# Performance work log

Hardware: AMD Instinct MI355X
Metric: run time of the kernel (lower is better)

Reference implementation:

```python
import jax, jax.numpy as jnp
import numpy as np

EPS = 1e-8
PAD = 1  # kernel // 2 for kernel=3


def setup_inputs() -> dict:
    key = jax.random.key(0)
    k1, k2, k3, k4, k5 = jax.random.split(key, 5)
    b, c, h, w = 16, 256, 64, 64
    out_ch, kernel, style_dim = 256, 3, 512
    x = jax.random.normal(k1, (b, c, h, w), dtype=jnp.float32)
    style = jax.random.normal(k2, (b, style_dim), dtype=jnp.float32)
    # learned params
    weight = jax.random.normal(k3, (1, out_ch, c, kernel, kernel), dtype=jnp.float32)
    lim = 1.0 / np.sqrt(style_dim)
    mod_w = jax.random.uniform(k4, (c, style_dim), minval=-lim, maxval=lim, dtype=jnp.float32)
    mod_b = jax.random.uniform(k5, (c,), minval=-lim, maxval=lim, dtype=jnp.float32)
    return {"x": x, "style": style, "weight": weight, "mod_w": mod_w, "mod_b": mod_b}


def reference(x, style, weight, mod_w, mod_b):
    # s[b,i]: per-sample, per-input-channel modulation from the style Linear
    s = style @ mod_w.T + mod_b                     # [b, in_ch]
    w = weight[0]                                    # [out_ch, in_ch, k, k]
    # demod factor: sum_{i,kh,kw} (w[o,i,kh,kw]*s[b,i])^2 = sum_i s^2 * sum_kk w^2
    w_sq = jnp.sum(w * w, axis=(2, 3))               # [out_ch, in_ch]
    d = jax.lax.rsqrt(jnp.einsum('oi,bi->bo', w_sq, s * s) + EPS)  # [b, out_ch]
    # modulate input channels instead of materializing per-sample weights
    xs = x * s[:, :, None, None]                     # [b, in_ch, h, w]
    y = jax.lax.conv_general_dilated(
        xs, w, window_strides=(1, 1), padding=[(PAD, PAD), (PAD, PAD)],
        dimension_numbers=('NCHW', 'OIHW', 'NCHW'))
    return y * d[:, :, None, None]                   # [b, out_ch, h, w]
```

## Files before the change

### kernel.cpp

```cpp
#include <hip/hip_runtime.h>
#include <hip/hip_bf16.h>
#include <cstdint>
#include <cstddef>

typedef __bf16 bf16_t;
typedef __bf16 bf16x4 __attribute__((ext_vector_type(4)));
typedef __bf16 bf16x8 __attribute__((ext_vector_type(8)));
typedef float  f32x4  __attribute__((ext_vector_type(4)));

#define NB   16
#define NC   256
#define NO   256
#define SD   512
#define NPIX 4096
#define CPAD 36

#define WS_S   0
#define WS_D   16384
#define WS_WSQ 32768
#define WS_WT  294912

__global__ __launch_bounds__(256) void prep1(
    const float* __restrict__ style, const float* __restrict__ weight,
    const float* __restrict__ mod_w, const float* __restrict__ mod_b,
    float* __restrict__ s_buf, float* __restrict__ wsq, bf16_t* __restrict__ wT)
{
    const int blk = blockIdx.x;
    const int tid = threadIdx.x;
    if (blk < 16) {
        const int b = blk, i = tid;
        const float* st = style + b * SD;
        const float* mw = mod_w + i * SD;
        float acc = 0.f;
        for (int k = 0; k < SD; k += 4) {
            float4 a = *(const float4*)(st + k);
            float4 c = *(const float4*)(mw + k);
            acc += a.x * c.x + a.y * c.y + a.z * c.z + a.w * c.w;
        }
        s_buf[b * NC + i] = acc + mod_b[i];
    } else {
        const int o = blk - 16, i = tid;
        const float* wp = weight + (o * NC + i) * 9;
        float q = 0.f;
        #pragma unroll
        for (int t = 0; t < 9; ++t) {
            float v = wp[t];
            q += v * v;
            wT[t * (NO * NC) + o * NC + i] = (bf16_t)v;
        }
        wsq[o * NC + i] = q;
    }
}

__global__ __launch_bounds__(256) void prep2(
    const float* __restrict__ s_buf, const float* __restrict__ wsq,
    float* __restrict__ d_buf)
{
    const int b = blockIdx.x, o = threadIdx.x;
    const float* wq = wsq + o * NC;
    const float* sb = s_buf + b * NC;
    float sum = 0.f;
    for (int i = 0; i < NC; ++i) {
        float sv = sb[i];
        sum += wq[i] * sv * sv;
    }
    d_buf[b * NC + o] = rsqrtf(sum + 1e-8f);
}

__device__ __forceinline__ void stage_a(const bf16_t* __restrict__ wT_tap,
                                        int o0, int ic0, bf16_t* dst, int tid)
{
    #pragma unroll
    for (int it = 0; it < 2; ++it) {
        int s = it * 256 + tid;
        const bf16_t* g = wT_tap + (o0 + (s >> 2)) * NC + ic0 + (s & 3) * 8;
        __builtin_amdgcn_global_load_lds(
            (const __attribute__((address_space(1))) void*)g,
            (__attribute__((address_space(3))) void*)(dst + s * 8),
            16, 0, 0);
    }
}

__global__ __launch_bounds__(256) void conv_mfma(
    const float* __restrict__ x,
    const bf16_t* __restrict__ wT,
    const float* __restrict__ s_buf,
    const float* __restrict__ d_buf,
    float* __restrict__ out)
{
    __shared__ bf16_t lds_a[2][128 * 32];
    __shared__ bf16_t lds_b[4 * 64 * CPAD];

    const int tid   = threadIdx.x;
    const int lane  = tid & 63;
    const int wv    = tid >> 6;
    const int wo    = wv >> 1;
    const int wp    = wv & 1;
    const int pt    = blockIdx.x;
    const int o0    = blockIdx.y * 128;
    const int batch = blockIdx.z;
    const int row0  = pt * 2;

    const int l15 = lane & 15;
    const int k0  = (lane >> 4) * 8;

    const int colB = tid & 63;
    const int cgrp = tid >> 6;

    f32x4 acc[4][4];
    #pragma unroll
    for (int i = 0; i < 4; ++i)
        #pragma unroll
        for (int j = 0; j < 4; ++j) {
            f32x4 z = {0.f, 0.f, 0.f, 0.f};
            acc[i][j] = z;
        }

    bf16x8 bzero;
    #pragma unroll
    for (int j = 0; j < 8; ++j) bzero[j] = (bf16_t)0.f;

    for (int chunk = 0; chunk < 8; ++chunk) {
        const int ic0 = chunk * 32;

        {
            float sv[8];
            #pragma unroll
            for (int c = 0; c < 8; ++c)
                sv[c] = s_buf[batch * NC + ic0 + cgrp * 8 + c];
            const float* xbase = x + (size_t)(batch * NC + ic0 + cgrp * 8) * NPIX + colB;
            #pragma unroll
            for (int r = 0; r < 4; ++r) {
                const int gy = row0 - 1 + r;
                const bool valid = ((unsigned)gy < 64u);
                const int lbase = (r * 64 + colB) * CPAD + cgrp * 8;
                #pragma unroll
                for (int cp = 0; cp < 4; ++cp) {
                    float v0 = 0.f, v1 = 0.f;
                    if (valid) {
                        v0 = xbase[(2 * cp)     * NPIX + gy * 64] * sv[2 * cp];
                        v1 = xbase[(2 * cp + 1) * NPIX + gy * 64] * sv[2 * cp + 1];
                    }
                    union { bf16_t h[2]; uint32_t u; } pk;
                    pk.h[0] = (bf16_t)v0;
                    pk.h[1] = (bf16_t)v1;
                    *(uint32_t*)&lds_b[lbase + 2 * cp] = pk.u;
                }
            }
        }
        stage_a(wT, o0, ic0, &lds_a[0][0], tid);
        __syncthreads();

        #pragma unroll
        for (int tap = 0; tap < 9; ++tap) {
            if (tap < 8)
                stage_a(wT + (tap + 1) * (NO * NC), o0, ic0,
                        &lds_a[(tap + 1) & 1][0], tid);

            const bf16_t* abuf = &lds_a[tap & 1][0];
            const int kh = tap / 3, kw = tap % 3;

            bf16x8 af[4];
            #pragma unroll
            for (int of = 0; of < 4; ++of)
                af[of] = *(const bf16x8*)&abuf[(wo * 64 + of * 16 + l15) * 32 + k0];

            const int r = wp + kh;
            bf16x8 bfr[4];
            #pragma unroll
            for (int nf = 0; nf < 4; ++nf) {
                const int c = nf * 16 + l15 + kw - 1;
                if ((unsigned)c < 64u) {
                    const bf16_t* p = &lds_b[(r * 64 + c) * CPAD + k0];
                    bf16x4 lo = *(const bf16x4*)p;
                    bf16x4 hi = *(const bf16x4*)(p + 4);
                    bfr[nf] = __builtin_shufflevector(lo, hi, 0, 1, 2, 3, 4, 5, 6, 7);
                } else {
                    bfr[nf] = bzero;
                }
            }

            #pragma unroll
            for (int of = 0; of < 4; ++of)
                #pragma unroll
                for (int nf = 0; nf < 4; ++nf)
                    acc[of][nf] = __builtin_amdgcn_mfma_f32_16x16x32_bf16(
                        af[of], bfr[nf], acc[of][nf], 0, 0, 0);

            __syncthreads();
        }
    }

    const int p_base = pt * 128 + wp * 64;
    #pragma unroll
    for (int of = 0; of < 4; ++of) {
        #pragma unroll
        for (int rg = 0; rg < 4; ++rg) {
            const int o_g = o0 + wo * 64 + of * 16 + (lane >> 4) * 4 + rg;
            const float dv = d_buf[batch * NO + o_g];
            const size_t obase = (size_t)(batch * NO + o_g) * NPIX;
            #pragma unroll
            for (int nf = 0; nf < 4; ++nf) {
                const int p_g = p_base + nf * 16 + l15;
                out[obase + p_g] = acc[of][nf][rg] * dv;
            }
        }
    }
}

extern "C" void kernel_launch(void* const* d_in, const int* in_sizes, int n_in,
                              void* d_out, int out_size, void* d_ws, size_t ws_size,
                              hipStream_t stream)
{
    const float* x      = (const float*)d_in[0];
    const float* style  = (const float*)d_in[1];
    const float* weight = (const float*)d_in[2];
    const float* mod_w  = (const float*)d_in[3];
    const float* mod_b  = (const float*)d_in[4];
    float* out = (float*)d_out;

    char* ws = (char*)d_ws;
    float*  s_buf = (float*)(ws + WS_S);
    float*  d_buf = (float*)(ws + WS_D);
    float*  wsq   = (float*)(ws + WS_WSQ);
    bf16_t* wT    = (bf16_t*)(ws + WS_WT);

    hipLaunchKernelGGL(prep1, dim3(272), dim3(256), 0, stream,
                       style, weight, mod_w, mod_b, s_buf, wsq, wT);
    hipLaunchKernelGGL(prep2, dim3(16), dim3(256), 0, stream, s_buf, wsq, d_buf);
    hipLaunchKernelGGL(conv_mfma, dim3(32, 2, 16), dim3(256), 0, stream,
                       x, wT, s_buf, d_buf, out);
}
```

Before: 262.8 us.

## Double pixel tile per block, swizzle LDS layouts, transpose wsq for coalesced prep2

Each conv block now covers 4 output rows instead of 2, so every staged weight tile feeds twice as many MFMAs and the grid halves. The LDS layouts for weights and activations get an XOR-style swizzle, and activation cells widen to 40 so each can be read with a single 16-byte load without bank conflicts. prep2 reads a transposed wsq with s^2 cached in shared memory so its loads coalesce. The accumulators double to 128 floats per thread, which raises register pressure, and the grid of 512 blocks gives less parallelism.

```diff
diff --git a/kernel.cpp b/kernel.cpp
--- a/kernel.cpp
+++ b/kernel.cpp
@@ -4,7 +4,6 @@
 #include <cstddef>
 
 typedef __bf16 bf16_t;
-typedef __bf16 bf16x4 __attribute__((ext_vector_type(4)));
 typedef __bf16 bf16x8 __attribute__((ext_vector_type(8)));
 typedef float  f32x4  __attribute__((ext_vector_type(4)));
 
@@ -13,7 +12,7 @@
 #define NO   256
 #define SD   512
 #define NPIX 4096
-#define CPAD 36
+#define CELL 40
 
 #define WS_S   0
 #define WS_D   16384
@@ -23,7 +22,7 @@
 __global__ __launch_bounds__(256) void prep1(
     const float* __restrict__ style, const float* __restrict__ weight,
     const float* __restrict__ mod_w, const float* __restrict__ mod_b,
-    float* __restrict__ s_buf, float* __restrict__ wsq, bf16_t* __restrict__ wT)
+    float* __restrict__ s_buf, float* __restrict__ wsqT, bf16_t* __restrict__ wT)
 {
     const int blk = blockIdx.x;
     const int tid = threadIdx.x;
@@ -41,29 +40,32 @@
     } else {
         const int o = blk - 16, i = tid;
         const float* wp = weight + (o * NC + i) * 9;
+        const int qi = (i >> 3) & 3;
+        const int f  = (o >> 1) & 3;
+        const int ci = (i & ~31) | ((((qi + f) & 3)) << 3) | (i & 7);
         float q = 0.f;
         #pragma unroll
         for (int t = 0; t < 9; ++t) {
             float v = wp[t];
             q += v * v;
-            wT[t * (NO * NC) + o * NC + i] = (bf16_t)v;
-        }
-        wsq[o * NC + i] = q;
+            wT[t * (NO * NC) + o * NC + ci] = (bf16_t)v;
+        }
+        wsqT[i * NO + o] = q;
     }
 }
 
 __global__ __launch_bounds__(256) void prep2(
-    const float* __restrict__ s_buf, const float* __restrict__ wsq,
+    const float* __restrict__ s_buf, const float* __restrict__ wsqT,
     float* __restrict__ d_buf)
 {
+    __shared__ float sh[NC];
     const int b = blockIdx.x, o = threadIdx.x;
-    const float* wq = wsq + o * NC;
-    const float* sb = s_buf + b * NC;
+    float sv = s_buf[b * NC + o];
+    sh[o] = sv * sv;
+    __syncthreads();
     float sum = 0.f;
-    for (int i = 0; i < NC; ++i) {
-        float sv = sb[i];
-        sum += wq[i] * sv * sv;
-    }
+    for (int i = 0; i < NC; ++i)
+        sum += wsqT[i * NO + o] * sh[i];
     d_buf[b * NC + o] = rsqrtf(sum + 1e-8f);
 }
 
@@ -81,7 +83,7 @@
     }
 }
 
-__global__ __launch_bounds__(256) void conv_mfma(
+__global__ __launch_bounds__(256, 2) void conv_mfma(
     const float* __restrict__ x,
     const bf16_t* __restrict__ wT,
     const float* __restrict__ s_buf,
@@ -89,7 +91,7 @@
     float* __restrict__ out)
 {
     __shared__ bf16_t lds_a[2][128 * 32];
-    __shared__ bf16_t lds_b[4 * 64 * CPAD];
+    __shared__ bf16_t lds_b[6 * 64 * CELL];
 
     const int tid   = threadIdx.x;
     const int lane  = tid & 63;
@@ -99,19 +101,21 @@
     const int pt    = blockIdx.x;
     const int o0    = blockIdx.y * 128;
     const int batch = blockIdx.z;
-    const int row0  = pt * 2;
+    const int row0  = pt * 4;
 
     const int l15 = lane & 15;
-    const int k0  = (lane >> 4) * 8;
+    const int q   = lane >> 4;
+    const int sAo = (((q + ((l15 >> 1) & 3)) & 3)) * 8;
 
     const int colB = tid & 63;
     const int cgrp = tid >> 6;
-
-    f32x4 acc[4][4];
+    const int sW   = ((cgrp + (colB >> 3)) & 3);
+
+    f32x4 acc[4][8];
     #pragma unroll
     for (int i = 0; i < 4; ++i)
         #pragma unroll
-        for (int j = 0; j < 4; ++j) {
+        for (int j = 0; j < 8; ++j) {
             f32x4 z = {0.f, 0.f, 0.f, 0.f};
             acc[i][j] = z;
         }
@@ -128,24 +132,23 @@
             #pragma unroll
             for (int c = 0; c < 8; ++c)
                 sv[c] = s_buf[batch * NC + ic0 + cgrp * 8 + c];
-            const float* xbase = x + (size_t)(batch * NC + ic0 + cgrp * 8) * NPIX + colB;
-            #pragma unroll
-            for (int r = 0; r < 4; ++r) {
+            const float* xb = x + (size_t)(batch * NC + ic0 + cgrp * 8) * NPIX + colB;
+            #pragma unroll
+            for (int r = 0; r < 6; ++r) {
                 const int gy = row0 - 1 + r;
                 const bool valid = ((unsigned)gy < 64u);
-                const int lbase = (r * 64 + colB) * CPAD + cgrp * 8;
+                bf16x8 pk;
                 #pragma unroll
                 for (int cp = 0; cp < 4; ++cp) {
                     float v0 = 0.f, v1 = 0.f;
                     if (valid) {
-                        v0 = xbase[(2 * cp)     * NPIX + gy * 64] * sv[2 * cp];
-                        v1 = xbase[(2 * cp + 1) * NPIX + gy * 64] * sv[2 * cp + 1];
+                        v0 = xb[(2 * cp)     * NPIX + gy * 64] * sv[2 * cp];
+                        v1 = xb[(2 * cp + 1) * NPIX + gy * 64] * sv[2 * cp + 1];
                     }
-                    union { bf16_t h[2]; uint32_t u; } pk;
-                    pk.h[0] = (bf16_t)v0;
-                    pk.h[1] = (bf16_t)v1;
-                    *(uint32_t*)&lds_b[lbase + 2 * cp] = pk.u;
+                    pk[2 * cp]     = (bf16_t)v0;
+                    pk[2 * cp + 1] = (bf16_t)v1;
                 }
+                *(bf16x8*)&lds_b[(r * 64 + colB) * CELL + sW * 8] = pk;
             }
         }
         stage_a(wT, o0, ic0, &lds_a[0][0], tid);
@@ -163,46 +166,40 @@
             bf16x8 af[4];
             #pragma unroll
             for (int of = 0; of < 4; ++of)
-                af[of] = *(const bf16x8*)&abuf[(wo * 64 + of * 16 + l15) * 32 + k0];
-
-            const int r = wp + kh;
-            bf16x8 bfr[4];
-            #pragma unroll
-            for (int nf = 0; nf < 4; ++nf) {
-                const int c = nf * 16 + l15 + kw - 1;
+                af[of] = *(const bf16x8*)&abuf[(wo * 64 + of * 16 + l15) * 32 + sAo];
+
+            #pragma unroll
+            for (int nf = 0; nf < 8; ++nf) {
+                const int r = wp * 2 + (nf >> 2) + kh;
+                const int c = (nf & 3) * 16 + l15 + kw - 1;
+                bf16x8 bfr;
                 if ((unsigned)c < 64u) {
-                    const bf16_t* p = &lds_b[(r * 64 + c) * CPAD + k0];
-                    bf16x4 lo = *(const bf16x4*)p;
-                    bf16x4 hi = *(const bf16x4*)(p + 4);
-                    bfr[nf] = __builtin_shufflevector(lo, hi, 0, 1, 2, 3, 4, 5, 6, 7);
+                    const int sB = (q + (c >> 3)) & 3;
+                    bfr = *(const bf16x8*)&lds_b[(r * 64 + c) * CELL + sB * 8];
                 } else {
-                    bfr[nf] = bzero;
+                    bfr = bzero;
                 }
+                #pragma unroll
+                for (int of = 0; of < 4; ++of)
+                    acc[of][nf] = __builtin_amdgcn_mfma_f32_16x16x32_bf16(
+                        af[of], bfr, acc[of][nf], 0, 0, 0);
             }
-
-            #pragma unroll
-            for (int of = 0; of < 4; ++of)
-                #pragma unroll
-                for (int nf = 0; nf < 4; ++nf)
-                    acc[of][nf] = __builtin_amdgcn_mfma_f32_16x16x32_bf16(
-                        af[of], bfr[nf], acc[of][nf], 0, 0, 0);
-
             __syncthreads();
         }
     }
 
-    const int p_base = pt * 128 + wp * 64;
     #pragma unroll
     for (int of = 0; of < 4; ++of) {
         #pragma unroll
         for (int rg = 0; rg < 4; ++rg) {
-            const int o_g = o0 + wo * 64 + of * 16 + (lane >> 4) * 4 + rg;
+            const int o_g = o0 + wo * 64 + of * 16 + q * 4 + rg;
             const float dv = d_buf[batch * NO + o_g];
-            const size_t obase = (size_t)(batch * NO + o_g) * NPIX;
-            #pragma unroll
-            for (int nf = 0; nf < 4; ++nf) {
-                const int p_g = p_base + nf * 16 + l15;
-                out[obase + p_g] = acc[of][nf][rg] * dv;
+            float* ob = out + ((size_t)(batch * NO + o_g) * 64 + row0) * 64;
+            #pragma unroll
+            for (int nf = 0; nf < 8; ++nf) {
+                const int rl  = wp * 2 + (nf >> 2);
+                const int col = (nf & 3) * 16 + l15;
+                ob[rl * 64 + col] = acc[of][nf][rg] * dv;
             }
         }
     }
@@ -222,12 +219,12 @@
     char* ws = (char*)d_ws;
     float*  s_buf = (float*)(ws + WS_S);
     float*  d_buf = (float*)(ws + WS_D);
-    float*  wsq   = (float*)(ws + WS_WSQ);
+    float*  wsqT  = (float*)(ws + WS_WSQ);
     bf16_t* wT    = (bf16_t*)(ws + WS_WT);
 
     hipLaunchKernelGGL(prep1, dim3(272), dim3(256), 0, stream,
-                       style, weight, mod_w, mod_b, s_buf, wsq, wT);
-    hipLaunchKernelGGL(prep2, dim3(16), dim3(256), 0, stream, s_buf, wsq, d_buf);
-    hipLaunchKernelGGL(conv_mfma, dim3(32, 2, 16), dim3(256), 0, stream,
+                       style, weight, mod_w, mod_b, s_buf, wsqT, wT);
+    hipLaunchKernelGGL(prep2, dim3(16), dim3(256), 0, stream, s_buf, wsqT, d_buf);
+    hipLaunchKernelGGL(conv_mfma, dim3(16, 2, 16), dim3(256), 0, stream,
                        x, wT, s_buf, d_buf, out);
 }
```

After: 315.0 us. +19.9%, slower.
